# Optimization experiments

Measured on AMD Instinct MI355X. Metric: run time of the kernel, lower is better.

Reference implementation:

```python
import jax, jax.numpy as jnp
import numpy as np
from jax import lax

STRIDES = (8, 16, 32)
NUM_CLASSES = 80
REG_MAX = 16
CONF_THR = 0.25
IOU_THR = 0.7
MAX_DET = 300
MAX_WH = 7680.0  # class-id offset for class-aware NMS


def setup_inputs() -> dict:
    key = jax.random.key(0)
    k1, k2, k3 = jax.random.split(key, 3)
    B = 32
    C = 4 * REG_MAX + NUM_CLASSES  # 144
    return {
        "p3": jax.random.normal(k1, (B, 80, 80, C), jnp.float32),
        "p4": jax.random.normal(k2, (B, 40, 40, C), jnp.float32),
        "p5": jax.random.normal(k3, (B, 20, 20, C), jnp.float32),
    }


def _make_anchors(shapes, strides):
    pts, strs = [], []
    for (h, w), s in zip(shapes, strides):
        sx = jnp.arange(w, dtype=jnp.float32) + 0.5
        sy = jnp.arange(h, dtype=jnp.float32) + 0.5
        gy, gx = jnp.meshgrid(sy, sx, indexing="ij")
        pts.append(jnp.stack([gx.ravel(), gy.ravel()], 0))  # (2, h*w)
        strs.append(jnp.full((h * w,), float(s), jnp.float32))
    return jnp.concatenate(pts, 1), jnp.concatenate(strs, 0)  # (2,A), (A,)


def _pairwise_iou(a, b):
    # a: (K,4) xyxy, b: (K,4) xyxy -> (K,K)
    lt = jnp.maximum(a[:, None, :2], b[None, :, :2])
    rb = jnp.minimum(a[:, None, 2:], b[None, :, 2:])
    wh = jnp.clip(rb - lt, 0.0)
    inter = wh[..., 0] * wh[..., 1]
    aa = (a[:, 2] - a[:, 0]) * (a[:, 3] - a[:, 1])
    ab = (b[:, 2] - b[:, 0]) * (b[:, 3] - b[:, 1])
    return inter / (aa[:, None] + ab[None, :] - inter + 1e-7)


def _nms_single(pred):
    # pred: (A, 4+nc) with boxes in xywh (center) format, scores sigmoid-activated
    xywh = pred[:, :4]
    scores = pred[:, 4:]
    best = jnp.max(scores, axis=-1)
    cls = jnp.argmax(scores, axis=-1)
    half = xywh[:, 2:] * 0.5
    boxes = jnp.concatenate([xywh[:, :2] - half, xywh[:, :2] + half], -1)  # xyxy
    score = jnp.where(best > CONF_THR, best, 0.0)
    top_s, idx = lax.top_k(score, MAX_DET)
    cbox = boxes[idx]                      # (K,4)
    ccls = cls[idx]                        # (K,)
    obox = cbox + ccls.astype(cbox.dtype)[:, None] * MAX_WH  # class-aware offset
    iou = _pairwise_iou(obox, obox)        # (K,K)
    k = jnp.arange(MAX_DET)

    def body(keep, i):
        suppressed = jnp.any(keep & (iou[i] > IOU_THR) & (k < i))
        ki = (top_s[i] > 0.0) & (~suppressed)
        return keep.at[i].set(ki), None

    keep, _ = lax.scan(body, jnp.zeros((MAX_DET,), bool), k)
    det = jnp.concatenate([cbox, top_s[:, None], ccls[:, None].astype(jnp.float32)], -1)
    return jnp.where(keep[:, None], det, 0.0)  # (K, 6): x1,y1,x2,y2,conf,cls


def _forward(p3, p4, p5):
    feats = [p3, p4, p5]
    shapes = [(f.shape[1], f.shape[2]) for f in feats]
    B = p3.shape[0]
    C = 4 * REG_MAX + NUM_CLASSES
    x = jnp.concatenate([f.reshape(B, -1, C) for f in feats], axis=1)  # (B, A, 144)
    box = x[:, :, : 4 * REG_MAX]   # (B, A, 64)
    cls = x[:, :, 4 * REG_MAX:]    # (B, A, 80)
    # DFL: split 64 channels into 4 sides x 16 bins, softmax over bins, expectation
    probs = jax.nn.softmax(box.reshape(B, -1, 4, REG_MAX), axis=-1)
    bins = jnp.arange(REG_MAX, dtype=jnp.float32)
    dist = jnp.einsum("bakr,r->bak", probs, bins)  # (B, A, 4) = l,t,r,b distances
    anchors, stride = _make_anchors(shapes, STRIDES)
    anc = anchors.T[None]  # (1, A, 2) anchor centers in grid units
    x1y1 = anc - dist[:, :, :2]
    x2y2 = anc + dist[:, :, 2:]
    dbox = jnp.concatenate([(x1y1 + x2y2) * 0.5, x2y2 - x1y1], -1) * stride[None, :, None]
    return jnp.concatenate([dbox, jax.nn.sigmoid(cls)], -1)  # (B, A, 84)


def reference(p3, p4, p5):
    pred = _forward(p3, p4, p5)
    return jax.vmap(_nms_single)(pred)  # (B, MAX_DET, 6)
```

## Files before the change

kernel.cpp:

```cpp
#include <hip/hip_runtime.h>
#include <math.h>

#define NUM_CLASSES 80
#define REG_MAX 16
#define NCH 144
#define A_TOT 8400
#define BATCH 32
#define MAX_DET 300
#define DET_PAD 320
#define CONF_THR 0.25f
#define IOU_THR 0.7f
#define MAX_WH 7680.0f
#define CAP 1024
#define NBINS 1024
#define MASK_W 10
#define MROW 324
#define NTRI 1760

__global__ __launch_bounds__(256) void score_kernel(
    const float* __restrict__ p3, const float* __restrict__ p4,
    const float* __restrict__ p5,
    float* __restrict__ scores, int* __restrict__ clsArr)
{
    const int t = blockIdx.x * 256 + threadIdx.x;
    const int g = t >> 2;
    const int p = t & 3;
    const int b = g / A_TOT;
    const int a = g - b * A_TOT;

    const float* src;
    if (a < 6400)      src = p3 + ((size_t)b * 6400 + a) * NCH;
    else if (a < 8000) src = p4 + ((size_t)b * 1600 + (a - 6400)) * NCH;
    else               src = p5 + ((size_t)b * 400  + (a - 8000)) * NCH;

    const float4* s4 = (const float4*)src;
    float best = -INFINITY;
    int cbest = p * 4;
    #pragma unroll
    for (int q = 0; q < 5; ++q) {
        float4 c4 = s4[16 + q * 4 + p];
        int c = q * 16 + p * 4;
        if (c4.x > best) { best = c4.x; cbest = c + 0; }
        if (c4.y > best) { best = c4.y; cbest = c + 1; }
        if (c4.z > best) { best = c4.z; cbest = c + 2; }
        if (c4.w > best) { best = c4.w; cbest = c + 3; }
    }
    #pragma unroll
    for (int d = 1; d < 4; d <<= 1) {
        float ob = __shfl_xor(best, d, 64);
        int   oc = __shfl_xor(cbest, d, 64);
        if (ob > best || (ob == best && oc < cbest)) { best = ob; cbest = oc; }
    }

    if (p == 0) {
        float sig = 1.0f / (1.0f + expf(-best));
        scores[g] = (sig > CONF_THR) ? sig : 0.0f;
        clsArr[g] = cbest;
    }
}

__global__ __launch_bounds__(1024, 4) void nms_fused_kernel(
    const float* __restrict__ p3, const float* __restrict__ p4,
    const float* __restrict__ p5,
    const float* __restrict__ scores, const int* __restrict__ clsArr,
    float* __restrict__ out)
{
    __shared__ float sc_l[A_TOT];
    __shared__ unsigned hist[NBINS];
    __shared__ unsigned wtot[16];
    __shared__ unsigned woff[16];
    __shared__ unsigned long long cand[CAP];
    __shared__ unsigned long long sortedK[MAX_DET];
    __shared__ float4 cbox4[MAX_DET];
    __shared__ float4 obox4[DET_PAD];
    __shared__ float oarea[DET_PAD];
    __shared__ float tops[MAX_DET];
    __shared__ float tcls[MAX_DET];
    __shared__ unsigned mask[MASK_W][MROW];
    __shared__ unsigned aliveW[MASK_W];
    __shared__ unsigned keepW[MASK_W];
    __shared__ int bstar;
    __shared__ unsigned cnt;

    const int b = blockIdx.x;
    const int tid = threadIdx.x;
    const int lane = tid & 63;
    const int wv = tid >> 6;
    const float* sc = scores + (size_t)b * A_TOT;
    const int* cl = clsArr + (size_t)b * A_TOT;

    hist[tid] = 0;
    if (tid < MAX_DET) sortedK[tid] = 0ULL;
    if (tid == 0) { cnt = 0u; bstar = 0; }
    __syncthreads();

    #pragma unroll
    for (int k = 0; k < 9; ++k) {
        int i = tid + k * 1024;
        if (i < A_TOT) {
            float s = sc[i];
            sc_l[i] = s;
            if (s > 0.0f) {
                int bin = min((int)(s * (float)NBINS), NBINS - 1);
                atomicAdd(&hist[bin], 1u);
            }
        }
    }
    __syncthreads();

    unsigned v = hist[tid];
    #pragma unroll
    for (int d = 1; d < 64; d <<= 1) {
        unsigned o = __shfl_down(v, d, 64);
        if (lane + d < 64) v += o;
    }
    if (lane == 0) wtot[wv] = v;
    __syncthreads();
    if (tid < 16) {
        unsigned u = wtot[tid];
        unsigned t2 = u;
        #pragma unroll
        for (int d = 1; d < 16; d <<= 1) {
            unsigned o = __shfl_down(t2, d, 64);
            if (tid + d < 16) t2 += o;
        }
        woff[tid] = t2 - u;
    }
    __syncthreads();
    unsigned suff = v + woff[wv];
    hist[tid] = suff;
    __syncthreads();

    if (hist[tid] >= MAX_DET && (tid == NBINS - 1 || hist[tid + 1] < MAX_DET))
        bstar = tid;
    __syncthreads();
    const int bs = bstar;

    #pragma unroll
    for (int k = 0; k < 9; ++k) {
        int i = tid + k * 1024;
        float s = (i < A_TOT) ? sc_l[i] : 0.0f;
        bool pass = false;
        if (s > 0.0f) {
            int bin = min((int)(s * (float)NBINS), NBINS - 1);
            pass = (bin >= bs);
        }
        unsigned long long mb = __ballot(pass);
        unsigned nw = (unsigned)__popcll(mb);
        unsigned base = 0u;
        if (lane == 0) base = nw ? atomicAdd(&cnt, nw) : 0u;
        base = __shfl(base, 0, 64);
        if (pass) {
            unsigned off = (unsigned)__popcll(mb & ((1ULL << lane) - 1ULL));
            unsigned pos = base + off;
            if (pos < CAP) {
                unsigned sb = __float_as_uint(s);
                cand[pos] = ((unsigned long long)sb << 32) |
                            (unsigned long long)(0xFFFFFFFFu - (unsigned)i);
            }
        }
    }
    __syncthreads();

    const int n = min((int)cnt, CAP);
    if (tid < n) {
        unsigned long long mykey = cand[tid];
        int r = 0;
        #pragma unroll 8
        for (int j = 0; j < n; ++j) r += (cand[j] > mykey) ? 1 : 0;
        if (r < MAX_DET) sortedK[r] = mykey;
    }
    __syncthreads();

    const int gbase = lane & ~3;
    #pragma unroll
    for (int sweep = 0; sweep < 2; ++sweep) {
        int det = sweep * 256 + (tid >> 2);
        int p = tid & 3;
        unsigned long long key = (det < MAX_DET) ? sortedK[det] : 0ULL;
        float distp = 0.0f;
        unsigned i = 0xFFFFFFFFu - (unsigned)(key & 0xFFFFFFFFull);

        if (key != 0ULL) {
            const float* rowp;
            if (i < 6400)      rowp = p3 + ((size_t)b * 6400 + i) * NCH;
            else if (i < 8000) rowp = p4 + ((size_t)b * 1600 + (i - 6400)) * NCH;
            else               rowp = p5 + ((size_t)b * 400  + (i - 8000)) * NCH;
            const float4* s4 = (const float4*)rowp;
            float vv[16];
            float4 r0 = s4[p * 4 + 0];
            float4 r1 = s4[p * 4 + 1];
            float4 r2 = s4[p * 4 + 2];
            float4 r3 = s4[p * 4 + 3];
            vv[0]=r0.x; vv[1]=r0.y; vv[2]=r0.z; vv[3]=r0.w;
            vv[4]=r1.x; vv[5]=r1.y; vv[6]=r1.z; vv[7]=r1.w;
            vv[8]=r2.x; vv[9]=r2.y; vv[10]=r2.z; vv[11]=r2.w;
            vv[12]=r3.x; vv[13]=r3.y; vv[14]=r3.z; vv[15]=r3.w;
            float m = vv[0];
            #pragma unroll
            for (int k2 = 1; k2 < 16; ++k2) m = fmaxf(m, vv[k2]);
            float ssum = 0.0f, wsum = 0.0f;
            #pragma unroll
            for (int k2 = 0; k2 < 16; ++k2) {
                float e = expf(vv[k2] - m);
                ssum += e;
                wsum += e * (float)k2;
            }
            distp = wsum / ssum;
        }
        float d0 = __shfl(distp, gbase + 0, 64);
        float d1 = __shfl(distp, gbase + 1, 64);
        float d2 = __shfl(distp, gbase + 2, 64);
        float d3 = __shfl(distp, gbase + 3, 64);

        if (det < MAX_DET && p == 0) {
            float s = __uint_as_float((unsigned)(key >> 32));
            tops[det] = s;
            float4 bb = make_float4(0.f, 0.f, 0.f, 0.f);
            float4 ob = bb;
            float cf = 0.0f;
            if (key != 0ULL) {
                int gyi, gxi; float strd;
                if (i < 6400)      { gyi = i / 80; gxi = i - gyi * 80; strd = 8.0f; }
                else if (i < 8000) { int li = i - 6400; gyi = li / 40; gxi = li - gyi * 40; strd = 16.0f; }
                else               { int li = i - 8000; gyi = li / 20; gxi = li - gyi * 20; strd = 32.0f; }
                float gx = (float)gxi + 0.5f;
                float gy = (float)gyi + 0.5f;
                float x1 = gx - d0, y1 = gy - d1;
                float x2 = gx + d2, y2 = gy + d3;
                float cx = ((x1 + x2) * 0.5f) * strd;
                float cy = ((y1 + y2) * 0.5f) * strd;
                float bw = (x2 - x1) * strd;
                float bh = (y2 - y1) * strd;
                float hx = bw * 0.5f, hy = bh * 0.5f;
                bb = make_float4(cx - hx, cy - hy, cx + hx, cy + hy);
                cf = (float)cl[i];
                float off = cf * MAX_WH;
                ob = make_float4(bb.x + off, bb.y + off, bb.z + off, bb.w + off);
            }
            cbox4[det] = bb;
            obox4[det] = ob;
            tcls[det] = cf;
            oarea[det] = (ob.z - ob.x) * (ob.w - ob.y);
        } else if (det >= MAX_DET && det < DET_PAD && p == 0) {
            obox4[det] = make_float4(0.f, 0.f, 0.f, 0.f);
            oarea[det] = 0.0f;
        }
    }
    __syncthreads();

    for (int t = tid; t < NTRI; t += 1024) {
        int w = (int)((sqrtf(16.0f + 4.0f * (float)t) - 4.0f) * 0.125f);
        while (16 * (w + 1) * (w + 2) <= t) ++w;
        while (16 * w * (w + 1) > t) --w;
        int i = t - 16 * w * (w + 1);
        const int j0 = w * 32;

        float4 a = obox4[i];
        float aa = oarea[i];
        unsigned bits = 0;
        #pragma unroll 8
        for (int jj = 0; jj < 32; ++jj) {
            int j = j0 + jj;
            float4 bo = obox4[j];
            float ab = oarea[j];
            float lx = fmaxf(a.x, bo.x), ly = fmaxf(a.y, bo.y);
            float rx = fminf(a.z, bo.z), ry = fminf(a.w, bo.w);
            float iw = fmaxf(rx - lx, 0.0f), ih = fmaxf(ry - ly, 0.0f);
            float inter = iw * ih;
            float iou = inter / (aa + ab - inter + 1e-7f);
            if (iou > IOU_THR) bits |= (1u << jj);
        }
        mask[w][i] = bits;
    }
    if (tid < MASK_W) {
        unsigned a = 0u;
        #pragma unroll
        for (int ii = 0; ii < 32; ++ii) {
            int i = tid * 32 + ii;
            if (i < MAX_DET && tops[i] > 0.0f) a |= (1u << ii);
        }
        aliveW[tid] = a;
    }
    __syncthreads();

    if (tid < 64) {
        unsigned supp = 0u;
        for (int w = 0; w < MASK_W; ++w) {
            unsigned suppcur = __shfl(supp, w, 64);
            unsigned aw = aliveW[w];
            unsigned m[32];
            #pragma unroll
            for (int q = 0; q < 8; ++q) {
                uint4 mq = *(const uint4*)&mask[w][w * 32 + q * 4];
                m[q*4+0] = mq.x; m[q*4+1] = mq.y;
                m[q*4+2] = mq.z; m[q*4+3] = mq.w;
            }
            unsigned kw = 0u;
            #pragma unroll
            for (int ii = 0; ii < 32; ++ii) {
                if (w * 32 + ii < MAX_DET) {
                    bool live = ((aw >> ii) & 1u) && !((suppcur >> ii) & 1u);
                    if (live) { suppcur |= m[ii]; kw |= (1u << ii); }
                }
            }
            if (tid == 0) keepW[w] = kw;
            if (tid < MASK_W) {
                unsigned acc = 0u;
                #pragma unroll
                for (int ii = 0; ii < 32; ++ii) {
                    if ((kw >> ii) & 1u) acc |= mask[tid][w * 32 + ii];
                }
                supp |= acc;
            }
        }
    }
    __syncthreads();

    float* ob = out + (size_t)b * MAX_DET * 6;
    for (int e = tid; e < MAX_DET * 6; e += 1024) {
        int i = e / 6, c = e - (e / 6) * 6;
        float val = 0.0f;
        if ((keepW[i >> 5] >> (i & 31)) & 1u) {
            if (c < 4)        val = (&cbox4[i].x)[c];
            else if (c == 4)  val = tops[i];
            else              val = tcls[i];
        }
        ob[e] = val;
    }
}

extern "C" void kernel_launch(void* const* d_in, const int* in_sizes, int n_in,
                              void* d_out, int out_size, void* d_ws, size_t ws_size,
                              hipStream_t stream) {
    const float* p3 = (const float*)d_in[0];
    const float* p4 = (const float*)d_in[1];
    const float* p5 = (const float*)d_in[2];
    float* out = (float*)d_out;

    char* base = (char*)d_ws;
    float* scores = (float*)base;
    int*   cls    = (int*)(base + 1075200);

    score_kernel<<<4200, 256, 0, stream>>>(p3, p4, p5, scores, cls);
    nms_fused_kernel<<<BATCH, 1024, 0, stream>>>(p3, p4, p5, scores, cls, out);
}
```

Baseline: 66.85 us.

## Move score histogram and candidate compaction out of the per-batch NMS block

The score histogram is now built with global atomics inside score_kernel. A new multi-block compact_kernel finds the threshold bin and compacts the candidates into a global buffer. Previously one 1024-thread block per image did the histogram, scan and compaction serially over 8400 scores while only 32 blocks occupied the GPU. The change adds a memset, an extra kernel launch, global atomic contention and a global round-trip for candidates.

After: 103.0 us. 54.0% more time.

```diff
diff --git a/kernel.cpp b/kernel.cpp
--- a/kernel.cpp
+++ b/kernel.cpp
@@ -16,11 +16,13 @@
 #define MASK_W 10
 #define MROW 324
 #define NTRI 1760
+#define BLK_PER_B 33
 
 __global__ __launch_bounds__(256) void score_kernel(
     const float* __restrict__ p3, const float* __restrict__ p4,
     const float* __restrict__ p5,
-    float* __restrict__ scores, int* __restrict__ clsArr)
+    float* __restrict__ scores, int* __restrict__ clsArr,
+    unsigned* __restrict__ ghist)
 {
     const int t = blockIdx.x * 256 + threadIdx.x;
     const int g = t >> 2;
@@ -54,21 +56,102 @@
 
     if (p == 0) {
         float sig = 1.0f / (1.0f + expf(-best));
-        scores[g] = (sig > CONF_THR) ? sig : 0.0f;
+        float s = (sig > CONF_THR) ? sig : 0.0f;
+        scores[g] = s;
         clsArr[g] = cbest;
+        if (s > 0.0f) {
+            int bin = min((int)(s * (float)NBINS), NBINS - 1);
+            atomicAdd(&ghist[b * NBINS + bin], 1u);
+        }
     }
 }
 
-__global__ __launch_bounds__(1024, 4) void nms_fused_kernel(
+__global__ __launch_bounds__(256) void compact_kernel(
+    const float* __restrict__ scores, const unsigned* __restrict__ ghist,
+    unsigned* __restrict__ gcnt, unsigned long long* __restrict__ gcand)
+{
+    __shared__ unsigned wtot[4];
+    __shared__ unsigned woffS[4];
+    __shared__ int bsSh;
+
+    const int bid = blockIdx.x;
+    const int b = bid / BLK_PER_B;
+    const int c = bid - b * BLK_PER_B;
+    const int tid = threadIdx.x;
+    const int lane = tid & 63;
+    const int wv = tid >> 6;
+
+    if (tid == 0) bsSh = 0;
+
+    uint4 h = *(const uint4*)&ghist[b * NBINS + 4 * tid];
+    unsigned s3 = h.w;
+    unsigned s2 = h.z + s3;
+    unsigned s1 = h.y + s2;
+    unsigned s0 = h.x + s1;
+    unsigned T = s0;
+    unsigned v = T;
+    #pragma unroll
+    for (int d = 1; d < 64; d <<= 1) {
+        unsigned o = __shfl_down(v, d, 64);
+        if (lane + d < 64) v += o;
+    }
+    if (lane == 0) wtot[wv] = v;
+    __syncthreads();
+    if (tid < 4) {
+        unsigned u = wtot[tid];
+        unsigned t2 = u;
+        #pragma unroll
+        for (int d = 1; d < 4; d <<= 1) {
+            unsigned o = __shfl_down(t2, d, 64);
+            if (tid + d < 4) t2 += o;
+        }
+        woffS[tid] = t2 - u;
+    }
+    __syncthreads();
+    unsigned E = (v - T) + woffS[wv];
+    unsigned sf0 = s0 + E, sf1 = s1 + E, sf2 = s2 + E, sf3 = s3 + E;
+    if (sf0 >= MAX_DET && sf1 < MAX_DET) bsSh = 4 * tid + 0;
+    if (sf1 >= MAX_DET && sf2 < MAX_DET) bsSh = 4 * tid + 1;
+    if (sf2 >= MAX_DET && sf3 < MAX_DET) bsSh = 4 * tid + 2;
+    if (sf3 >= MAX_DET && E   < MAX_DET) bsSh = 4 * tid + 3;
+    __syncthreads();
+    const int bs = bsSh;
+
+    const int a = c * 256 + tid;
+    bool pass = false;
+    float s = 0.0f;
+    if (a < A_TOT) {
+        s = scores[(size_t)b * A_TOT + a];
+        if (s > 0.0f) {
+            int bin = min((int)(s * (float)NBINS), NBINS - 1);
+            pass = (bin >= bs);
+        }
+    }
+    unsigned long long mb = __ballot(pass);
+    unsigned nw = (unsigned)__popcll(mb);
+    unsigned basep = 0u;
+    if (lane == 0 && nw) basep = atomicAdd(&gcnt[b * 32], nw);
+    basep = __shfl(basep, 0, 64);
+    if (pass) {
+        unsigned off = (unsigned)__popcll(mb & ((1ULL << lane) - 1ULL));
+        unsigned pos = basep + off;
+        if (pos < CAP) {
+            unsigned sb = __float_as_uint(s);
+            gcand[(size_t)b * CAP + pos] =
+                ((unsigned long long)sb << 32) |
+                (unsigned long long)(0xFFFFFFFFu - (unsigned)a);
+        }
+    }
+}
+
+__global__ __launch_bounds__(1024, 4) void nms_kernel(
     const float* __restrict__ p3, const float* __restrict__ p4,
     const float* __restrict__ p5,
-    const float* __restrict__ scores, const int* __restrict__ clsArr,
+    const int* __restrict__ clsArr,
+    const unsigned* __restrict__ gcnt,
+    const unsigned long long* __restrict__ gcand,
     float* __restrict__ out)
 {
-    __shared__ float sc_l[A_TOT];
-    __shared__ unsigned hist[NBINS];
-    __shared__ unsigned wtot[16];
-    __shared__ unsigned woff[16];
     __shared__ unsigned long long cand[CAP];
     __shared__ unsigned long long sortedK[MAX_DET];
     __shared__ float4 cbox4[MAX_DET];
@@ -79,96 +162,25 @@
     __shared__ unsigned mask[MASK_W][MROW];
     __shared__ unsigned aliveW[MASK_W];
     __shared__ unsigned keepW[MASK_W];
-    __shared__ int bstar;
-    __shared__ unsigned cnt;
 
     const int b = blockIdx.x;
     const int tid = threadIdx.x;
     const int lane = tid & 63;
-    const int wv = tid >> 6;
-    const float* sc = scores + (size_t)b * A_TOT;
     const int* cl = clsArr + (size_t)b * A_TOT;
 
-    hist[tid] = 0;
+    const int n = min((int)gcnt[b * 32], CAP);
+    cand[tid] = (tid < n) ? gcand[(size_t)b * CAP + tid] : 0ULL;
     if (tid < MAX_DET) sortedK[tid] = 0ULL;
-    if (tid == 0) { cnt = 0u; bstar = 0; }
-    __syncthreads();
-
-    #pragma unroll
-    for (int k = 0; k < 9; ++k) {
-        int i = tid + k * 1024;
-        if (i < A_TOT) {
-            float s = sc[i];
-            sc_l[i] = s;
-            if (s > 0.0f) {
-                int bin = min((int)(s * (float)NBINS), NBINS - 1);
-                atomicAdd(&hist[bin], 1u);
-            }
-        }
-    }
-    __syncthreads();
-
-    unsigned v = hist[tid];
-    #pragma unroll
-    for (int d = 1; d < 64; d <<= 1) {
-        unsigned o = __shfl_down(v, d, 64);
-        if (lane + d < 64) v += o;
-    }
-    if (lane == 0) wtot[wv] = v;
-    __syncthreads();
-    if (tid < 16) {
-        unsigned u = wtot[tid];
-        unsigned t2 = u;
-        #pragma unroll
-        for (int d = 1; d < 16; d <<= 1) {
-            unsigned o = __shfl_down(t2, d, 64);
-            if (tid + d < 16) t2 += o;
-        }
-        woff[tid] = t2 - u;
-    }
-    __syncthreads();
-    unsigned suff = v + woff[wv];
-    hist[tid] = suff;
-    __syncthreads();
-
-    if (hist[tid] >= MAX_DET && (tid == NBINS - 1 || hist[tid + 1] < MAX_DET))
-        bstar = tid;
-    __syncthreads();
-    const int bs = bstar;
-
-    #pragma unroll
-    for (int k = 0; k < 9; ++k) {
-        int i = tid + k * 1024;
-        float s = (i < A_TOT) ? sc_l[i] : 0.0f;
-        bool pass = false;
-        if (s > 0.0f) {
-            int bin = min((int)(s * (float)NBINS), NBINS - 1);
-            pass = (bin >= bs);
-        }
-        unsigned long long mb = __ballot(pass);
-        unsigned nw = (unsigned)__popcll(mb);
-        unsigned base = 0u;
-        if (lane == 0) base = nw ? atomicAdd(&cnt, nw) : 0u;
-        base = __shfl(base, 0, 64);
-        if (pass) {
-            unsigned off = (unsigned)__popcll(mb & ((1ULL << lane) - 1ULL));
-            unsigned pos = base + off;
-            if (pos < CAP) {
-                unsigned sb = __float_as_uint(s);
-                cand[pos] = ((unsigned long long)sb << 32) |
-                            (unsigned long long)(0xFFFFFFFFu - (unsigned)i);
-            }
-        }
-    }
-    __syncthreads();
-
-    const int n = min((int)cnt, CAP);
+    __syncthreads();
+
     if (tid < n) {
         unsigned long long mykey = cand[tid];
-        int r = 0;
-        #pragma unroll 8
-        for (int j = 0; j < n; ++j) r += (cand[j] > mykey) ? 1 : 0;
-        if (r < MAX_DET) sortedK[r] = mykey;
+        if (mykey != 0ULL) {
+            int r = 0;
+            #pragma unroll 8
+            for (int j = 0; j < n; ++j) r += (cand[j] > mykey) ? 1 : 0;
+            if (r < MAX_DET) sortedK[r] = mykey;
+        }
     }
     __syncthreads();
 
@@ -339,9 +351,15 @@
     float* out = (float*)d_out;
 
     char* base = (char*)d_ws;
-    float* scores = (float*)base;
-    int*   cls    = (int*)(base + 1075200);
-
-    score_kernel<<<4200, 256, 0, stream>>>(p3, p4, p5, scores, cls);
-    nms_fused_kernel<<<BATCH, 1024, 0, stream>>>(p3, p4, p5, scores, cls, out);
+    float*              scores = (float*)base;
+    int*                cls    = (int*)(base + 1075200);
+    unsigned*           ghist  = (unsigned*)(base + 2150400);
+    unsigned*           gcnt   = (unsigned*)(base + 2281472);
+    unsigned long long* gcand  = (unsigned long long*)(base + 2285568);
+
+    hipMemsetAsync(ghist, 0, 131072 + 4096, stream);
+
+    score_kernel<<<4200, 256, 0, stream>>>(p3, p4, p5, scores, cls, ghist);
+    compact_kernel<<<BATCH * BLK_PER_B, 256, 0, stream>>>(scores, ghist, gcnt, gcand);
+    nms_kernel<<<BATCH, 1024, 0, stream>>>(p3, p4, p5, cls, gcnt, gcand, out);
 }
```
